# Kernel optimization log

Hardware: AMD Instinct MI355X
Metric: run time of the kernel (lower is better)

Reference implementation:

```python
import jax, jax.numpy as jnp
import numpy as np

B, L, DIM, H, HD = 2, 2048, 1024, 16, 64


def _rope_tables(L, hd):
    inv_freq = 1.0 / (10000.0 ** (np.arange(0, hd, 2, dtype=np.float32) / hd))
    t = np.arange(L, dtype=np.float32)
    freqs = np.outer(t, inv_freq)                 # [L, hd/2]
    emb = np.concatenate([freqs, freqs], axis=-1)  # [L, hd]
    return jnp.asarray(np.cos(emb)), jnp.asarray(np.sin(emb))


def setup_inputs() -> dict:
    key = jax.random.key(0)
    k1, k2, k3 = jax.random.split(key, 3)
    x = jax.random.normal(k1, (B, L, DIM), dtype=jnp.float32)
    cos, sin = _rope_tables(L, HD)
    w_qkv = jax.random.normal(k2, (DIM, 3 * H * HD), dtype=jnp.float32) * (DIM ** -0.5)
    w_out = jax.random.normal(k3, (H * HD, DIM), dtype=jnp.float32) * ((H * HD) ** -0.5)
    return {"x": x, "cos": cos, "sin": sin, "w_qkv": w_qkv, "w_out": w_out}


def _rotate_half(u):
    u1, u2 = jnp.split(u, 2, axis=-1)
    return jnp.concatenate([-u2, u1], axis=-1)


def _apply_rope(u, cos, sin):
    # u: [B, L, H, hd]; cos/sin: [L, hd]
    c = cos[None, :, None, :]
    s = sin[None, :, None, :]
    return u * c + _rotate_half(u) * s


def reference(x, cos, sin, w_qkv, w_out):
    b, l, _ = x.shape
    qkv = jnp.einsum('bld,de->ble', x, w_qkv).reshape(b, l, 3 * H, HD)
    q, k, v = jnp.split(qkv, 3, axis=2)          # each [B, L, H, hd]
    q = _apply_rope(q, cos, sin)
    k = _apply_rope(k, cos, sin)
    scale = HD ** -0.5                            # SDPA default scale
    scores = jnp.einsum('bqhd,bkhd->bhqk', q, k) * scale
    attn = jax.nn.softmax(scores, axis=-1)
    o = jnp.einsum('bhqk,bkhd->bqhd', attn, v).reshape(b, l, H * HD)
    return jnp.einsum('ble,ed->bld', o, w_out)
```

## Files before the change

### kernel.cpp

```cpp
#include <hip/hip_runtime.h>
#include <hip/hip_bf16.h>

#define BATCH 2
#define SEQ   2048
#define DIM   1024
#define NH    16
#define HD    64
#define K_DIM 1024

typedef __attribute__((ext_vector_type(8))) short short8;
typedef __attribute__((ext_vector_type(4))) short short4v;
typedef __attribute__((ext_vector_type(4))) float f32x4;
typedef unsigned short ushort_t;

__device__ __forceinline__ unsigned short f2b(float x) {
    unsigned int u = __float_as_uint(x);
    u += 0x7FFFu + ((u >> 16) & 1u);
    return (unsigned short)(u >> 16);
}

#define ASYNC_COPY16(gp, lp) \
    __builtin_amdgcn_global_load_lds((const __attribute__((address_space(1))) void*)(gp), \
                                     (__attribute__((address_space(3))) void*)(lp), 16, 0, 0)

__global__ __launch_bounds__(256)
void prep(const float* __restrict__ x, const float* __restrict__ w_qkv,
          const float* __restrict__ w_out, ushort_t* __restrict__ xb,
          ushort_t* __restrict__ wqb, ushort_t* __restrict__ wob)
{
    const int bid = blockIdx.x;
    if (bid < 1024) {
        constexpr int n4 = (BATCH * SEQ * DIM) / 4;
        int i = bid * 256 + threadIdx.x;
        for (; i < n4; i += 1024 * 256) {
            float4 v = ((const float4*)x)[i];
            short4v o;
            o[0] = (short)f2b(v.x); o[1] = (short)f2b(v.y);
            o[2] = (short)f2b(v.z); o[3] = (short)f2b(v.w);
            ((short4v*)xb)[i] = o;
        }
    } else {
        const int lane = threadIdx.x & 63;
        const float* src; ushort_t* dst; int N, job;
        if (bid < 2560) { src = w_qkv; dst = wqb; N = 3072; job = (bid - 1024) * 4 + (threadIdx.x >> 6); }
        else            { src = w_out; dst = wob; N = 1024; job = (bid - 2560) * 4 + (threadIdx.x >> 6); }
        const int jn = (N == 3072) ? (job % 48) : (job % 16);
        const int jk = (N == 3072) ? (job / 48) : (job / 16);
        const int n  = jn * 64 + lane;
        const int k0 = jk * 8;
        short8 o;
        #pragma unroll
        for (int j = 0; j < 8; ++j) o[j] = (short)f2b(src[(size_t)(k0 + j) * N + n]);
        *(short8*)(dst + (size_t)n * K_DIM + k0) = o;
    }
}

__device__ __forceinline__ void gemm_stage(const ushort_t* __restrict__ Ag,
                                           const ushort_t* __restrict__ Bg,
                                           ushort_t* As, ushort_t* Bs,
                                           int k0, int w, int r0, int c0)
{
    ASYNC_COPY16(Ag + (size_t)r0 * K_DIM + k0 + c0 * 8,        As + w * 512);
    ASYNC_COPY16(Ag + (size_t)(64 + r0) * K_DIM + k0 + c0 * 8, As + w * 512 + 2048);
    ASYNC_COPY16(Bg + (size_t)r0 * K_DIM + k0 + c0 * 8,        Bs + w * 512);
    ASYNC_COPY16(Bg + (size_t)(64 + r0) * K_DIM + k0 + c0 * 8, Bs + w * 512 + 2048);
}

__device__ __forceinline__ void mfma_gemm_tile(
    const ushort_t* __restrict__ Ag, const ushort_t* __restrict__ Bg,
    ushort_t (&As)[2][128 * 32], ushort_t (&Bs)[2][128 * 32], f32x4 acc[4][4])
{
    const int t = threadIdx.x;
    const int w = t >> 6, lane = t & 63;
    const int qd = lane >> 4, cl = lane & 15;
    const int p0 = w * 64 + lane;
    const int r0 = p0 >> 2;
    const int c0 = (p0 & 3) ^ (r0 & 3);

    gemm_stage(Ag, Bg, As[0], Bs[0], 0, w, r0, c0);

    for (int kt = 0; kt < K_DIM / 32; ++kt) {
        const int cur = kt & 1;
        __syncthreads();
        if (kt + 1 < K_DIM / 32)
            gemm_stage(Ag, Bg, As[cur ^ 1], Bs[cur ^ 1], (kt + 1) * 32, w, r0, c0);

        short8 af[4], bfr[4];
        #pragma unroll
        for (int rt = 0; rt < 4; ++rt) {
            const int row = (w >> 1) * 64 + rt * 16 + cl;
            af[rt] = *(const short8*)(As[cur] + row * 32 + ((qd ^ (row & 3)) * 8));
        }
        #pragma unroll
        for (int ct = 0; ct < 4; ++ct) {
            const int col = (w & 1) * 64 + ct * 16 + cl;
            bfr[ct] = *(const short8*)(Bs[cur] + col * 32 + ((qd ^ (col & 3)) * 8));
        }
        #pragma unroll
        for (int rt = 0; rt < 4; ++rt)
            #pragma unroll
            for (int ct = 0; ct < 4; ++ct)
                acc[rt][ct] = __builtin_amdgcn_mfma_f32_16x16x32_bf16(
                    af[rt], bfr[ct], acc[rt][ct], 0, 0, 0);
    }
}

__global__ __launch_bounds__(256, 3)
void gemm_qkv_mfma(const ushort_t* __restrict__ xb, const ushort_t* __restrict__ wqb,
                   ushort_t* __restrict__ qb, ushort_t* __restrict__ kb,
                   ushort_t* __restrict__ vt,
                   const float* __restrict__ cosb, const float* __restrict__ sinb)
{
    __shared__ __align__(16) ushort_t As[2][128 * 32];
    __shared__ __align__(16) ushort_t Bs[2][128 * 32];
    const int m0 = blockIdx.y * 128, n0 = blockIdx.x * 128;

    f32x4 acc[4][4];
    #pragma unroll
    for (int i = 0; i < 4; ++i)
        #pragma unroll
        for (int j = 0; j < 4; ++j)
            #pragma unroll
            for (int r = 0; r < 4; ++r) acc[i][j][r] = 0.f;

    mfma_gemm_tile(xb + (size_t)m0 * K_DIM, wqb + (size_t)n0 * K_DIM, As, Bs, acc);

    const int t = threadIdx.x, w = t >> 6, lane = t & 63;
    const int qd = lane >> 4, cl = lane & 15;
    const int b = m0 >> 11;
    const int lbase = (m0 & 2047) + (w >> 1) * 64;
    const int region = blockIdx.x >> 3;
    const int h = (blockIdx.x & 7) * 2 + (w & 1);

    if (region < 2) {
        ushort_t* dst = region ? kb : qb;
        const float sc = region ? 1.0f : 0.18033688011111234f;
        #pragma unroll
        for (int rt = 0; rt < 4; ++rt) {
            #pragma unroll
            for (int r = 0; r < 4; ++r) {
                const int l = lbase + rt * 16 + qd * 4 + r;
                const float c0 = cosb[l * HD + cl],      s0 = sinb[l * HD + cl];
                const float c1 = cosb[l * HD + 16 + cl], s1 = sinb[l * HD + 16 + cl];
                const float v0 = acc[rt][0][r] * c0 - acc[rt][2][r] * s0;
                const float v1 = acc[rt][1][r] * c1 - acc[rt][3][r] * s1;
                const float v2 = acc[rt][2][r] * c0 + acc[rt][0][r] * s0;
                const float v3 = acc[rt][3][r] * c1 + acc[rt][1][r] * s1;
                short4v o4;
                o4[0] = (short)f2b(v0 * sc);
                o4[1] = (short)f2b(v1 * sc);
                o4[2] = (short)f2b(v2 * sc);
                o4[3] = (short)f2b(v3 * sc);
                *(short4v*)(dst + (((size_t)b * NH + h) * SEQ + l) * HD + cl * 4) = o4;
            }
        }
    } else {
        #pragma unroll
        for (int rt = 0; rt < 4; ++rt)
            #pragma unroll
            for (int ct = 0; ct < 4; ++ct) {
                const int d = ct * 16 + cl;
                const int l = lbase + rt * 16 + qd * 4;
                short4v o4;
                #pragma unroll
                for (int r = 0; r < 4; ++r) o4[r] = (short)f2b(acc[rt][ct][r]);
                *(short4v*)(vt + (((size_t)b * NH + h) * HD + d) * SEQ + l) = o4;
            }
    }
}

__device__ __forceinline__ void go_stage(const ushort_t* __restrict__ Ag,
                                         const ushort_t* __restrict__ Bg,
                                         ushort_t* As, ushort_t* Bs,
                                         int k0, int w, int lane)
{
    #pragma unroll
    for (int j = 0; j < 2; ++j) {
        const int r = w * 32 + j * 16 + (lane >> 2);
        const int c = (lane & 3) ^ (r & 3);
        ASYNC_COPY16(Ag + (size_t)r * K_DIM + k0 + c * 8, As + (w * 128 + j * 64) * 8);
    }
    const int rb = w * 16 + (lane >> 2);
    const int cb = (lane & 3) ^ (rb & 3);
    ASYNC_COPY16(Bg + (size_t)rb * K_DIM + k0 + cb * 8, Bs + (w * 64) * 8);
}

__global__ __launch_bounds__(256, 3)
void gemm_out_mfma(const ushort_t* __restrict__ ob, const ushort_t* __restrict__ wob,
                   float* __restrict__ out)
{
    __shared__ __align__(16) ushort_t As[2][128 * 32];
    __shared__ __align__(16) ushort_t Bs[2][64 * 32];
    const int m0 = blockIdx.y * 128, n0 = blockIdx.x * 64;
    const int t = threadIdx.x;
    const int w = t >> 6, lane = t & 63;
    const int qd = lane >> 4, cl = lane & 15;
    const int wr = w >> 1, wc = w & 1;

    f32x4 acc[4][2];
    #pragma unroll
    for (int i = 0; i < 4; ++i)
        #pragma unroll
        for (int j = 0; j < 2; ++j)
            #pragma unroll
            for (int r = 0; r < 4; ++r) acc[i][j][r] = 0.f;

    const ushort_t* Ag = ob  + (size_t)m0 * K_DIM;
    const ushort_t* Bg = wob + (size_t)n0 * K_DIM;
    go_stage(Ag, Bg, As[0], Bs[0], 0, w, lane);

    for (int kt = 0; kt < K_DIM / 32; ++kt) {
        const int cur = kt & 1;
        __syncthreads();
        if (kt + 1 < K_DIM / 32)
            go_stage(Ag, Bg, As[cur ^ 1], Bs[cur ^ 1], (kt + 1) * 32, w, lane);

        short8 af[4], bfr[2];
        #pragma unroll
        for (int rt = 0; rt < 4; ++rt) {
            const int row = wr * 64 + rt * 16 + cl;
            af[rt] = *(const short8*)(As[cur] + row * 32 + ((qd ^ (row & 3)) * 8));
        }
        #pragma unroll
        for (int ct = 0; ct < 2; ++ct) {
            const int col = wc * 32 + ct * 16 + cl;
            bfr[ct] = *(const short8*)(Bs[cur] + col * 32 + ((qd ^ (col & 3)) * 8));
        }
        #pragma unroll
        for (int rt = 0; rt < 4; ++rt)
            #pragma unroll
            for (int ct = 0; ct < 2; ++ct)
                acc[rt][ct] = __builtin_amdgcn_mfma_f32_16x16x32_bf16(
                    af[rt], bfr[ct], acc[rt][ct], 0, 0, 0);
    }

    const int mbase = m0 + wr * 64, nbase = n0 + wc * 32;
    #pragma unroll
    for (int rt = 0; rt < 4; ++rt)
        #pragma unroll
        for (int ct = 0; ct < 2; ++ct)
            #pragma unroll
            for (int r = 0; r < 4; ++r)
                out[(size_t)(mbase + rt * 16 + qd * 4 + r) * DIM + nbase + ct * 16 + cl] =
                    acc[rt][ct][r];
}

__global__ __launch_bounds__(256, 3)
void attn_mfma(const ushort_t* __restrict__ qb, const ushort_t* __restrict__ kb,
               const ushort_t* __restrict__ vt, ushort_t* __restrict__ ob)
{
    const int h = blockIdx.x;
    const int b = blockIdx.y;
    const int qt = blockIdx.z;
    const int t = threadIdx.x;
    const int w = t >> 6, lane = t & 63;
    const int qd = lane >> 4, cl = lane & 15;
    constexpr int NT = SEQ / 64;

    __shared__ __align__(16) ushort_t Ks[2][64 * 64];
    __shared__ __align__(16) ushort_t Vs[2][64 * 64];
    __shared__ __align__(16) ushort_t P[4][2048];
    char* Pb = (char*)P[w];

    const size_t bh = (size_t)b * NH + h;
    const ushort_t* qbase = qb + (bh * SEQ + qt * 128 + w * 32) * HD;
    const ushort_t* kbase = kb + bh * SEQ * HD;
    const ushort_t* vbase = vt + bh * (size_t)HD * SEQ;

    const int p0 = w * 128 + lane;
    const int r0a = p0 >> 3,  c0a = (p0 & 7) ^ (r0a & 7);
    const int p1 = p0 + 64;
    const int r1a = p1 >> 3,  c1a = (p1 & 7) ^ (r1a & 7);
    const int ldsoff0 = (w * 128) * 8;
    const int ldsoff1 = (w * 128 + 64) * 8;

    short8 qf[2][2];
    #pragma unroll
    for (int nt = 0; nt < 2; ++nt)
        #pragma unroll
        for (int kh = 0; kh < 2; ++kh)
            qf[nt][kh] = *(const short8*)(qbase + (nt * 16 + cl) * HD + kh * 32 + qd * 8);

    f32x4 oaccT[4][2];
    float l_part[2] = {0.f, 0.f};
    #pragma unroll
    for (int dt = 0; dt < 4; ++dt)
        #pragma unroll
        for (int nt = 0; nt < 2; ++nt)
            #pragma unroll
            for (int r = 0; r < 4; ++r) oaccT[dt][nt][r] = 0.f;

    short8 pf_prev[2][2], vf_prev[4][2];
    #pragma unroll
    for (int nt = 0; nt < 2; ++nt)
        #pragma unroll
        for (int kh = 0; kh < 2; ++kh)
            #pragma unroll
            for (int e = 0; e < 8; ++e) pf_prev[nt][kh][e] = 0;
    #pragma unroll
    for (int dt = 0; dt < 4; ++dt)
        #pragma unroll
        for (int kh = 0; kh < 2; ++kh)
            #pragma unroll
            for (int e = 0; e < 8; ++e) vf_prev[dt][kh][e] = 0;

    {
        ASYNC_COPY16(kbase + (size_t)r0a * HD + c0a * 8,            (ushort_t*)Ks[0] + ldsoff0);
        ASYNC_COPY16(kbase + (size_t)r1a * HD + c1a * 8,            (ushort_t*)Ks[0] + ldsoff1);
        ASYNC_COPY16(vbase + (size_t)r0a * SEQ + c0a * 8,           (ushort_t*)Vs[0] + ldsoff0);
        ASYNC_COPY16(vbase + (size_t)r1a * SEQ + c1a * 8,           (ushort_t*)Vs[0] + ldsoff1);
    }

    for (int kt = 0; kt < NT; ++kt) {
        const int cur = kt & 1;
        __syncthreads();
        if (kt + 1 < NT) {
            const int g = kt + 1;
            ASYNC_COPY16(kbase + (size_t)(g * 64 + r0a) * HD + c0a * 8, (ushort_t*)Ks[cur ^ 1] + ldsoff0);
            ASYNC_COPY16(kbase + (size_t)(g * 64 + r1a) * HD + c1a * 8, (ushort_t*)Ks[cur ^ 1] + ldsoff1);
            ASYNC_COPY16(vbase + (size_t)r0a * SEQ + g * 64 + c0a * 8,  (ushort_t*)Vs[cur ^ 1] + ldsoff0);
            ASYNC_COPY16(vbase + (size_t)r1a * SEQ + g * 64 + c1a * 8,  (ushort_t*)Vs[cur ^ 1] + ldsoff1);
        }

        short8 kf[4][2], vf[4][2];
        #pragma unroll
        for (int mt = 0; mt < 4; ++mt)
            #pragma unroll
            for (int kh = 0; kh < 2; ++kh)
                kf[mt][kh] = *(const short8*)(Ks[cur] + ((mt * 16 + cl) * 8 + ((kh * 4 + qd) ^ (cl & 7))) * 8);
        #pragma unroll
        for (int dt = 0; dt < 4; ++dt)
            #pragma unroll
            for (int kh = 0; kh < 2; ++kh)
                vf[dt][kh] = *(const short8*)(Vs[cur] + ((dt * 16 + cl) * 8 + ((kh * 4 + qd) ^ (cl & 7))) * 8);

        f32x4 s[4][2];
        #pragma unroll
        for (int mt = 0; mt < 4; ++mt)
            #pragma unroll
            for (int nt = 0; nt < 2; ++nt)
                #pragma unroll
                for (int r = 0; r < 4; ++r) s[mt][nt][r] = 0.f;
        #pragma unroll
        for (int kh = 0; kh < 2; ++kh)
            #pragma unroll
            for (int mt = 0; mt < 4; ++mt)
                #pragma unroll
                for (int nt = 0; nt < 2; ++nt)
                    s[mt][nt] = __builtin_amdgcn_mfma_f32_16x16x32_bf16(
                        kf[mt][kh], qf[nt][kh], s[mt][nt], 0, 0, 0);

        #pragma unroll
        for (int kh = 0; kh < 2; ++kh)
            #pragma unroll
            for (int dt = 0; dt < 4; ++dt)
                #pragma unroll
                for (int nt = 0; nt < 2; ++nt)
                    oaccT[dt][nt] = __builtin_amdgcn_mfma_f32_16x16x32_bf16(
                        vf_prev[dt][kh], pf_prev[nt][kh], oaccT[dt][nt], 0, 0, 0);

        #pragma unroll
        for (int nt = 0; nt < 2; ++nt) {
            #pragma unroll
            for (int mt = 0; mt < 4; ++mt) {
                const float e0 = __builtin_amdgcn_exp2f(s[mt][nt][0]);
                const float e1 = __builtin_amdgcn_exp2f(s[mt][nt][1]);
                const float e2 = __builtin_amdgcn_exp2f(s[mt][nt][2]);
                const float e3 = __builtin_amdgcn_exp2f(s[mt][nt][3]);
                l_part[nt] += (e0 + e1) + (e2 + e3);
                union { __hip_bfloat162 h2[2]; unsigned long long u64; } pk;
                pk.h2[0] = __float22bfloat162_rn(make_float2(e0, e1));
                pk.h2[1] = __float22bfloat162_rn(make_float2(e2, e3));
                const int g = (mt * 2 + (qd >> 1)) ^ (cl & 7);
                *(unsigned long long*)(Pb + (nt * 16 + cl) * 128 + g * 16 + (qd & 1) * 8) = pk.u64;
            }
        }
        __builtin_amdgcn_wave_barrier();

        #pragma unroll
        for (int nt = 0; nt < 2; ++nt)
            #pragma unroll
            for (int kh = 0; kh < 2; ++kh)
                pf_prev[nt][kh] = *(const short8*)(Pb + (nt * 16 + cl) * 128 + (((kh * 4 + qd) ^ (cl & 7)) * 16));
        #pragma unroll
        for (int dt = 0; dt < 4; ++dt)
            #pragma unroll
            for (int kh = 0; kh < 2; ++kh)
                vf_prev[dt][kh] = vf[dt][kh];
    }

    #pragma unroll
    for (int kh = 0; kh < 2; ++kh)
        #pragma unroll
        for (int dt = 0; dt < 4; ++dt)
            #pragma unroll
            for (int nt = 0; nt < 2; ++nt)
                oaccT[dt][nt] = __builtin_amdgcn_mfma_f32_16x16x32_bf16(
                    vf_prev[dt][kh], pf_prev[nt][kh], oaccT[dt][nt], 0, 0, 0);

    #pragma unroll
    for (int nt = 0; nt < 2; ++nt) {
        float l = l_part[nt];
        l += __shfl_xor(l, 16);
        l += __shfl_xor(l, 32);
        const float inv = 1.0f / l;
        const int query = qt * 128 + w * 32 + nt * 16 + cl;
        ushort_t* op = ob + ((size_t)b * SEQ + query) * DIM + h * HD;
        #pragma unroll
        for (int dt = 0; dt < 4; ++dt) {
            short4v o4;
            #pragma unroll
            for (int r = 0; r < 4; ++r) o4[r] = (short)f2b(oaccT[dt][nt][r] * inv);
            *(short4v*)(op + dt * 16 + qd * 4) = o4;
        }
    }
}

extern "C" void kernel_launch(void* const* d_in, const int* in_sizes, int n_in,
                              void* d_out, int out_size, void* d_ws, size_t ws_size,
                              hipStream_t stream)
{
    const float* x     = (const float*)d_in[0];
    const float* cosb  = (const float*)d_in[1];
    const float* sinb  = (const float*)d_in[2];
    const float* w_qkv = (const float*)d_in[3];
    const float* w_out = (const float*)d_in[4];
    float* out = (float*)d_out;

    constexpr size_t MB = 1u << 20;
    char* ws = (char*)d_ws;
    ushort_t* qb  = (ushort_t*)(ws);
    ushort_t* kb  = (ushort_t*)(ws + 8 * MB);
    ushort_t* vt  = (ushort_t*)(ws + 16 * MB);
    ushort_t* wob = (ushort_t*)(ws + 24 * MB);
    ushort_t* ob  = (ushort_t*)(ws + 26 * MB);
    ushort_t* xb  = (ushort_t*)(ws + 34 * MB);
    ushort_t* wqb = (ushort_t*)(ws + 42 * MB);

    prep<<<3072, 256, 0, stream>>>(x, w_qkv, w_out, xb, wqb, wob);
    gemm_qkv_mfma<<<dim3(24, 32), 256, 0, stream>>>(xb, wqb, qb, kb, vt, cosb, sinb);
    attn_mfma<<<dim3(16, 2, 16), 256, 0, stream>>>(qb, kb, vt, ob);
    gemm_out_mfma<<<dim3(16, 32), 256, 0, stream>>>(ob, wob, out);
}
```

Before: 201.4 us.

## Repack softmax P via permlane swaps instead of LDS round-trip in attention

Removes the per-wave LDS scratch buffer used to transpose the bf16 probability tile into MFMA operand layout, and builds the operand registers directly with v_permlane32_swap and v_permlane16_swap cross-lane exchanges. This cuts LDS stores and loads plus a wave barrier per KV tile and lowers LDS usage. It also raises wave priority around the MFMA block and lowers the launch-bounds occupancy hint from 3 to 2, which gives the compiler more registers per thread but allows fewer resident blocks. If the permlane mapping does not exactly reproduce the old LDS layout, the attention output will be wrong.

```diff
diff --git a/kernel.cpp b/kernel.cpp
--- a/kernel.cpp
+++ b/kernel.cpp
@@ -245,7 +245,7 @@
                     acc[rt][ct][r];
 }
 
-__global__ __launch_bounds__(256, 3)
+__global__ __launch_bounds__(256, 2)
 void attn_mfma(const ushort_t* __restrict__ qb, const ushort_t* __restrict__ kb,
                const ushort_t* __restrict__ vt, ushort_t* __restrict__ ob)
 {
@@ -259,8 +259,6 @@
 
     __shared__ __align__(16) ushort_t Ks[2][64 * 64];
     __shared__ __align__(16) ushort_t Vs[2][64 * 64];
-    __shared__ __align__(16) ushort_t P[4][2048];
-    char* Pb = (char*)P[w];
 
     const size_t bh = (size_t)b * NH + h;
     const ushort_t* qbase = qb + (bh * SEQ + qt * 128 + w * 32) * HD;
@@ -341,6 +339,7 @@
             for (int nt = 0; nt < 2; ++nt)
                 #pragma unroll
                 for (int r = 0; r < 4; ++r) s[mt][nt][r] = 0.f;
+        __builtin_amdgcn_s_setprio(1);
         #pragma unroll
         for (int kh = 0; kh < 2; ++kh)
             #pragma unroll
@@ -358,9 +357,11 @@
                 for (int nt = 0; nt < 2; ++nt)
                     oaccT[dt][nt] = __builtin_amdgcn_mfma_f32_16x16x32_bf16(
                         vf_prev[dt][kh], pf_prev[nt][kh], oaccT[dt][nt], 0, 0, 0);
+        __builtin_amdgcn_s_setprio(0);
 
         #pragma unroll
         for (int nt = 0; nt < 2; ++nt) {
+            unsigned int wr[4][2];
             #pragma unroll
             for (int mt = 0; mt < 4; ++mt) {
                 const float e0 = __builtin_amdgcn_exp2f(s[mt][nt][0]);
@@ -368,20 +369,27 @@
                 const float e2 = __builtin_amdgcn_exp2f(s[mt][nt][2]);
                 const float e3 = __builtin_amdgcn_exp2f(s[mt][nt][3]);
                 l_part[nt] += (e0 + e1) + (e2 + e3);
-                union { __hip_bfloat162 h2[2]; unsigned long long u64; } pk;
-                pk.h2[0] = __float22bfloat162_rn(make_float2(e0, e1));
-                pk.h2[1] = __float22bfloat162_rn(make_float2(e2, e3));
-                const int g = (mt * 2 + (qd >> 1)) ^ (cl & 7);
-                *(unsigned long long*)(Pb + (nt * 16 + cl) * 128 + g * 16 + (qd & 1) * 8) = pk.u64;
+                union { __hip_bfloat162 h2; unsigned int u; } pk0, pk1;
+                pk0.h2 = __float22bfloat162_rn(make_float2(e0, e1));
+                pk1.h2 = __float22bfloat162_rn(make_float2(e2, e3));
+                wr[mt][0] = pk0.u;
+                wr[mt][1] = pk1.u;
             }
-        }
-        __builtin_amdgcn_wave_barrier();
-
-        #pragma unroll
-        for (int nt = 0; nt < 2; ++nt)
-            #pragma unroll
-            for (int kh = 0; kh < 2; ++kh)
-                pf_prev[nt][kh] = *(const short8*)(Pb + (nt * 16 + cl) * 128 + (((kh * 4 + qd) ^ (cl & 7)) * 16));
+            #pragma unroll
+            for (int kh = 0; kh < 2; ++kh) {
+                union { unsigned int u[4]; short8 s8; } pu;
+                #pragma unroll
+                for (int i = 0; i < 2; ++i) {
+                    unsigned int a  = wr[2 * kh][i];
+                    unsigned int bb = wr[2 * kh + 1][i];
+                    asm("v_permlane32_swap_b32 %0, %1" : "+v"(a), "+v"(bb));
+                    asm("v_permlane16_swap_b32 %0, %1" : "+v"(a), "+v"(bb));
+                    pu.u[i]     = a;
+                    pu.u[2 + i] = bb;
+                }
+                pf_prev[nt][kh] = pu.s8;
+            }
+        }
         #pragma unroll
         for (int dt = 0; dt < 4; ++dt)
             #pragma unroll
```

Result: faster. 191.0 us (-5.2%).

## Restructure attention pipeline with register-only P, MFMA row sums, and deeper K/V staging

Applied to the files above, without the earlier changes.

The attention kernel now stages K/V two 64-key tiles at a time into four LDS buffers and processes them in unrolled pairs. Exp results are kept in registers via permlane swaps instead of round-tripping through LDS, and softmax denominators are accumulated with an MFMA against a ones vector. The QK and PV MFMAs run at raised wave priority. The GEMM loops are unrolled by two with precomputed LDS fragment pointers to cut address arithmetic. These changes raise LDS and register use, so occupancy drops from three to two blocks per CU, and the tighter schedule is harder to verify as correct.

```diff
diff --git a/kernel.cpp b/kernel.cpp
--- a/kernel.cpp
+++ b/kernel.cpp
@@ -77,31 +77,53 @@
     const int r0 = p0 >> 2;
     const int c0 = (p0 & 3) ^ (r0 & 3);
 
+    const ushort_t* aB[4];
+    const ushort_t* bB[4];
+    #pragma unroll
+    for (int rt = 0; rt < 4; ++rt) {
+        const int row = (w >> 1) * 64 + rt * 16 + cl;
+        aB[rt] = As[0] + row * 32 + ((qd ^ (row & 3)) * 8);
+    }
+    #pragma unroll
+    for (int ct = 0; ct < 4; ++ct) {
+        const int col = (w & 1) * 64 + ct * 16 + cl;
+        bB[ct] = Bs[0] + col * 32 + ((qd ^ (col & 3)) * 8);
+    }
+
     gemm_stage(Ag, Bg, As[0], Bs[0], 0, w, r0, c0);
 
-    for (int kt = 0; kt < K_DIM / 32; ++kt) {
-        const int cur = kt & 1;
+    for (int kp = 0; kp < K_DIM / 64; ++kp) {
         __syncthreads();
-        if (kt + 1 < K_DIM / 32)
-            gemm_stage(Ag, Bg, As[cur ^ 1], Bs[cur ^ 1], (kt + 1) * 32, w, r0, c0);
-
-        short8 af[4], bfr[4];
-        #pragma unroll
-        for (int rt = 0; rt < 4; ++rt) {
-            const int row = (w >> 1) * 64 + rt * 16 + cl;
-            af[rt] = *(const short8*)(As[cur] + row * 32 + ((qd ^ (row & 3)) * 8));
-        }
-        #pragma unroll
-        for (int ct = 0; ct < 4; ++ct) {
-            const int col = (w & 1) * 64 + ct * 16 + cl;
-            bfr[ct] = *(const short8*)(Bs[cur] + col * 32 + ((qd ^ (col & 3)) * 8));
-        }
-        #pragma unroll
-        for (int rt = 0; rt < 4; ++rt)
-            #pragma unroll
-            for (int ct = 0; ct < 4; ++ct)
-                acc[rt][ct] = __builtin_amdgcn_mfma_f32_16x16x32_bf16(
-                    af[rt], bfr[ct], acc[rt][ct], 0, 0, 0);
+        gemm_stage(Ag, Bg, As[1], Bs[1], kp * 64 + 32, w, r0, c0);
+        {
+            short8 af[4], bfr[4];
+            #pragma unroll
+            for (int rt = 0; rt < 4; ++rt) af[rt] = *(const short8*)(aB[rt]);
+            #pragma unroll
+            for (int ct = 0; ct < 4; ++ct) bfr[ct] = *(const short8*)(bB[ct]);
+            #pragma unroll
+            for (int rt = 0; rt < 4; ++rt)
+                #pragma unroll
+                for (int ct = 0; ct < 4; ++ct)
+                    acc[rt][ct] = __builtin_amdgcn_mfma_f32_16x16x32_bf16(
+                        af[rt], bfr[ct], acc[rt][ct], 0, 0, 0);
+        }
+        __syncthreads();
+        if (kp + 1 < K_DIM / 64)
+            gemm_stage(Ag, Bg, As[0], Bs[0], kp * 64 + 64, w, r0, c0);
+        {
+            short8 af[4], bfr[4];
+            #pragma unroll
+            for (int rt = 0; rt < 4; ++rt) af[rt] = *(const short8*)(aB[rt] + 4096);
+            #pragma unroll
+            for (int ct = 0; ct < 4; ++ct) bfr[ct] = *(const short8*)(bB[ct] + 4096);
+            #pragma unroll
+            for (int rt = 0; rt < 4; ++rt)
+                #pragma unroll
+                for (int ct = 0; ct < 4; ++ct)
+                    acc[rt][ct] = __builtin_amdgcn_mfma_f32_16x16x32_bf16(
+                        af[rt], bfr[ct], acc[rt][ct], 0, 0, 0);
+        }
     }
 }
 
@@ -207,31 +229,54 @@
 
     const ushort_t* Ag = ob  + (size_t)m0 * K_DIM;
     const ushort_t* Bg = wob + (size_t)n0 * K_DIM;
+
+    const ushort_t* aB[4];
+    const ushort_t* bB[2];
+    #pragma unroll
+    for (int rt = 0; rt < 4; ++rt) {
+        const int row = wr * 64 + rt * 16 + cl;
+        aB[rt] = As[0] + row * 32 + ((qd ^ (row & 3)) * 8);
+    }
+    #pragma unroll
+    for (int ct = 0; ct < 2; ++ct) {
+        const int col = wc * 32 + ct * 16 + cl;
+        bB[ct] = Bs[0] + col * 32 + ((qd ^ (col & 3)) * 8);
+    }
+
     go_stage(Ag, Bg, As[0], Bs[0], 0, w, lane);
 
-    for (int kt = 0; kt < K_DIM / 32; ++kt) {
-        const int cur = kt & 1;
+    for (int kp = 0; kp < K_DIM / 64; ++kp) {
         __syncthreads();
-        if (kt + 1 < K_DIM / 32)
-            go_stage(Ag, Bg, As[cur ^ 1], Bs[cur ^ 1], (kt + 1) * 32, w, lane);
-
-        short8 af[4], bfr[2];
-        #pragma unroll
-        for (int rt = 0; rt < 4; ++rt) {
-            const int row = wr * 64 + rt * 16 + cl;
-            af[rt] = *(const short8*)(As[cur] + row * 32 + ((qd ^ (row & 3)) * 8));
-        }
-        #pragma unroll
-        for (int ct = 0; ct < 2; ++ct) {
-            const int col = wc * 32 + ct * 16 + cl;
-            bfr[ct] = *(const short8*)(Bs[cur] + col * 32 + ((qd ^ (col & 3)) * 8));
-        }
-        #pragma unroll
-        for (int rt = 0; rt < 4; ++rt)
-            #pragma unroll
-            for (int ct = 0; ct < 2; ++ct)
-                acc[rt][ct] = __builtin_amdgcn_mfma_f32_16x16x32_bf16(
-                    af[rt], bfr[ct], acc[rt][ct], 0, 0, 0);
+        go_stage(Ag, Bg, As[1], Bs[1], kp * 64 + 32, w, lane);
+        {
+            short8 af[4], bfr[2];
+            #pragma unroll
+            for (int rt = 0; rt < 4; ++rt) af[rt] = *(const short8*)(aB[rt]);
+            #pragma unroll
+            for (int ct = 0; ct < 2; ++ct) bfr[ct] = *(const short8*)(bB[ct]);
+            #pragma unroll
+            for (int rt = 0; rt < 4; ++rt)
+                #pragma unroll
+                for (int ct = 0; ct < 2; ++ct)
+                    acc[rt][ct] = __builtin_amdgcn_mfma_f32_16x16x32_bf16(
+                        af[rt], bfr[ct], acc[rt][ct], 0, 0, 0);
+        }
+        __syncthreads();
+        if (kp + 1 < K_DIM / 64)
+            go_stage(Ag, Bg, As[0], Bs[0], kp * 64 + 64, w, lane);
+        {
+            short8 af[4], bfr[2];
+            #pragma unroll
+            for (int rt = 0; rt < 4; ++rt) af[rt] = *(const short8*)(aB[rt] + 4096);
+            #pragma unroll
+            for (int ct = 0; ct < 2; ++ct) bfr[ct] = *(const short8*)(bB[ct] + 2048);
+            #pragma unroll
+            for (int rt = 0; rt < 4; ++rt)
+                #pragma unroll
+                for (int ct = 0; ct < 2; ++ct)
+                    acc[rt][ct] = __builtin_amdgcn_mfma_f32_16x16x32_bf16(
+                        af[rt], bfr[ct], acc[rt][ct], 0, 0, 0);
+        }
     }
 
     const int mbase = m0 + wr * 64, nbase = n0 + wc * 32;
@@ -245,7 +290,111 @@
                     acc[rt][ct][r];
 }
 
-__global__ __launch_bounds__(256, 3)
+#define QK_MFMA(kfv, sdst)                                                      \
+    _Pragma("unroll")                                                           \
+    for (int mt = 0; mt < 4; ++mt)                                              \
+        _Pragma("unroll")                                                       \
+        for (int nt = 0; nt < 2; ++nt)                                          \
+            sdst[mt][nt] = __builtin_amdgcn_mfma_f32_16x16x32_bf16(             \
+                kfv[mt][0], qf[nt][0], fz, 0, 0, 0);                            \
+    _Pragma("unroll")                                                           \
+    for (int mt = 0; mt < 4; ++mt)                                              \
+        _Pragma("unroll")                                                       \
+        for (int nt = 0; nt < 2; ++nt)                                          \
+            sdst[mt][nt] = __builtin_amdgcn_mfma_f32_16x16x32_bf16(             \
+                kfv[mt][1], qf[nt][1], sdst[mt][nt], 0, 0, 0);
+
+#define PV_MFMA(vfv, pfv)                                                       \
+    _Pragma("unroll")                                                           \
+    for (int kh = 0; kh < 2; ++kh)                                              \
+        _Pragma("unroll")                                                       \
+        for (int dt = 0; dt < 4; ++dt)                                          \
+            _Pragma("unroll")                                                   \
+            for (int nt = 0; nt < 2; ++nt)                                      \
+                oaccT[dt][nt] = __builtin_amdgcn_mfma_f32_16x16x32_bf16(        \
+                    vfv[dt][kh], pfv[nt][kh], oaccT[dt][nt], 0, 0, 0);
+
+#define L_MFMA(pfv)                                                             \
+    _Pragma("unroll")                                                           \
+    for (int kh = 0; kh < 2; ++kh)                                              \
+        _Pragma("unroll")                                                       \
+        for (int nt = 0; nt < 2; ++nt)                                          \
+            lacc[nt] = __builtin_amdgcn_mfma_f32_16x16x32_bf16(                 \
+                onesA, pfv[nt][kh], lacc[nt], 0, 0, 0);
+
+#define EXPPACK(sv, pfD)                                                        \
+    _Pragma("unroll")                                                           \
+    for (int nt = 0; nt < 2; ++nt) {                                            \
+        unsigned int wr2[4][2];                                                 \
+        _Pragma("unroll")                                                       \
+        for (int mt = 0; mt < 4; ++mt) {                                        \
+            const float e0 = __builtin_amdgcn_exp2f(sv[mt][nt][0]);             \
+            const float e1 = __builtin_amdgcn_exp2f(sv[mt][nt][1]);             \
+            const float e2 = __builtin_amdgcn_exp2f(sv[mt][nt][2]);             \
+            const float e3 = __builtin_amdgcn_exp2f(sv[mt][nt][3]);             \
+            union { __hip_bfloat162 h2; unsigned int u; } pk0, pk1;             \
+            pk0.h2 = __float22bfloat162_rn(make_float2(e0, e1));                \
+            pk1.h2 = __float22bfloat162_rn(make_float2(e2, e3));                \
+            wr2[mt][0] = pk0.u;                                                 \
+            wr2[mt][1] = pk1.u;                                                 \
+        }                                                                       \
+        _Pragma("unroll")                                                       \
+        for (int kh = 0; kh < 2; ++kh) {                                        \
+            union { unsigned int u[4]; short8 s8; } pu;                         \
+            _Pragma("unroll")                                                   \
+            for (int i = 0; i < 2; ++i) {                                       \
+                unsigned int a  = wr2[2 * kh][i];                               \
+                unsigned int bb = wr2[2 * kh + 1][i];                           \
+                asm("v_permlane32_swap_b32 %0, %1" : "+v"(a), "+v"(bb));        \
+                asm("v_permlane16_swap_b32 %0, %1" : "+v"(a), "+v"(bb));        \
+                pu.u[i]     = a;                                                \
+                pu.u[2 + i] = bb;                                               \
+            }                                                                   \
+            pfD[nt][kh] = pu.s8;                                                \
+        }                                                                       \
+    }
+
+#define PAIR_BODY(BOFF, pfC, vfC, pfP, vfP)                                     \
+    {                                                                           \
+        short8 kf[4][2], vfT[4][2], pfT[2][2];                                  \
+        f32x4 s[4][2];                                                          \
+                                                          \
+        _Pragma("unroll")                                                       \
+        for (int mt = 0; mt < 4; ++mt) {                                        \
+            kf[mt][0] = *(const short8*)(kb0 + (BOFF) + mt * 1024);             \
+            kf[mt][1] = *(const short8*)(kb1 + (BOFF) + mt * 1024);             \
+        }                                                                       \
+        _Pragma("unroll")                                                       \
+        for (int dt = 0; dt < 4; ++dt) {                                        \
+            vfT[dt][0] = *(const short8*)(vb0 + (BOFF) + dt * 1024);            \
+            vfT[dt][1] = *(const short8*)(vb1 + (BOFF) + dt * 1024);            \
+        }                                                                       \
+        __builtin_amdgcn_s_setprio(1);                                          \
+        QK_MFMA(kf, s)                                                          \
+        PV_MFMA(vfC, pfC)                                                       \
+        __builtin_amdgcn_s_setprio(0);                                          \
+        EXPPACK(s, pfT)                                                         \
+        L_MFMA(pfT)                                                             \
+                                                          \
+        _Pragma("unroll")                                                       \
+        for (int mt = 0; mt < 4; ++mt) {                                        \
+            kf[mt][0] = *(const short8*)(kb0 + (BOFF) + 4096 + mt * 1024);      \
+            kf[mt][1] = *(const short8*)(kb1 + (BOFF) + 4096 + mt * 1024);      \
+        }                                                                       \
+        _Pragma("unroll")                                                       \
+        for (int dt = 0; dt < 4; ++dt) {                                        \
+            vfP[dt][0] = *(const short8*)(vb0 + (BOFF) + 4096 + dt * 1024);     \
+            vfP[dt][1] = *(const short8*)(vb1 + (BOFF) + 4096 + dt * 1024);     \
+        }                                                                       \
+        __builtin_amdgcn_s_setprio(1);                                          \
+        QK_MFMA(kf, s)                                                          \
+        PV_MFMA(vfT, pfT)                                                       \
+        __builtin_amdgcn_s_setprio(0);                                          \
+        EXPPACK(s, pfP)                                                         \
+        L_MFMA(pfP)                                                             \
+    }
+
+__global__ __launch_bounds__(256, 2)
 void attn_mfma(const ushort_t* __restrict__ qb, const ushort_t* __restrict__ kb,
                const ushort_t* __restrict__ vt, ushort_t* __restrict__ ob)
 {
@@ -255,12 +404,9 @@
     const int t = threadIdx.x;
     const int w = t >> 6, lane = t & 63;
     const int qd = lane >> 4, cl = lane & 15;
-    constexpr int NT = SEQ / 64;
-
-    __shared__ __align__(16) ushort_t Ks[2][64 * 64];
-    __shared__ __align__(16) ushort_t Vs[2][64 * 64];
-    __shared__ __align__(16) ushort_t P[4][2048];
-    char* Pb = (char*)P[w];
+
+    __shared__ __align__(16) ushort_t Ks[4][64 * 64];
+    __shared__ __align__(16) ushort_t Vs[4][64 * 64];
 
     const size_t bh = (size_t)b * NH + h;
     const ushort_t* qbase = qb + (bh * SEQ + qt * 128 + w * 32) * HD;
@@ -274,6 +420,16 @@
     const int ldsoff0 = (w * 128) * 8;
     const int ldsoff1 = (w * 128 + 64) * 8;
 
+    const ushort_t* kg0 = kbase + (size_t)r0a * HD + c0a * 8;
+    const ushort_t* kg1 = kbase + (size_t)r1a * HD + c1a * 8;
+    const ushort_t* vg0 = vbase + (size_t)r0a * SEQ + c0a * 8;
+    const ushort_t* vg1 = vbase + (size_t)r1a * SEQ + c1a * 8;
+
+    const int lo0 = (cl * 8 + (qd ^ (cl & 7))) * 8;
+    const int lo1 = (cl * 8 + ((4 + qd) ^ (cl & 7))) * 8;
+    const ushort_t* kb0 = Ks[0] + lo0; const ushort_t* kb1 = Ks[0] + lo1;
+    const ushort_t* vb0 = Vs[0] + lo0; const ushort_t* vb1 = Vs[0] + lo1;
+
     short8 qf[2][2];
     #pragma unroll
     for (int nt = 0; nt < 2; ++nt)
@@ -281,129 +437,85 @@
         for (int kh = 0; kh < 2; ++kh)
             qf[nt][kh] = *(const short8*)(qbase + (nt * 16 + cl) * HD + kh * 32 + qd * 8);
 
+    const f32x4 fz = {0.f, 0.f, 0.f, 0.f};
+    short8 onesA;
+    #pragma unroll
+    for (int e = 0; e < 8; ++e) onesA[e] = (short)0x3F80;
+
     f32x4 oaccT[4][2];
-    float l_part[2] = {0.f, 0.f};
+    f32x4 lacc[2];
     #pragma unroll
     for (int dt = 0; dt < 4; ++dt)
         #pragma unroll
         for (int nt = 0; nt < 2; ++nt)
             #pragma unroll
             for (int r = 0; r < 4; ++r) oaccT[dt][nt][r] = 0.f;
-
-    short8 pf_prev[2][2], vf_prev[4][2];
     #pragma unroll
     for (int nt = 0; nt < 2; ++nt)
         #pragma unroll
+        for (int r = 0; r < 4; ++r) lacc[nt][r] = 0.f;
+
+    short8 pf01[2][2], vf01[4][2], pf23[2][2], vf23[4][2];
+    #pragma unroll
+    for (int nt = 0; nt < 2; ++nt)
+        #pragma unroll
         for (int kh = 0; kh < 2; ++kh)
             #pragma unroll
-            for (int e = 0; e < 8; ++e) pf_prev[nt][kh][e] = 0;
+            for (int e = 0; e < 8; ++e) pf23[nt][kh][e] = 0;
     #pragma unroll
     for (int dt = 0; dt < 4; ++dt)
         #pragma unroll
         for (int kh = 0; kh < 2; ++kh)
             #pragma unroll
-            for (int e = 0; e < 8; ++e) vf_prev[dt][kh][e] = 0;
+            for (int e = 0; e < 8; ++e) vf23[dt][kh][e] = 0;
 
     {
-        ASYNC_COPY16(kbase + (size_t)r0a * HD + c0a * 8,            (ushort_t*)Ks[0] + ldsoff0);
-        ASYNC_COPY16(kbase + (size_t)r1a * HD + c1a * 8,            (ushort_t*)Ks[0] + ldsoff1);
-        ASYNC_COPY16(vbase + (size_t)r0a * SEQ + c0a * 8,           (ushort_t*)Vs[0] + ldsoff0);
-        ASYNC_COPY16(vbase + (size_t)r1a * SEQ + c1a * 8,           (ushort_t*)Vs[0] + ldsoff1);
-    }
-
-    for (int kt = 0; kt < NT; ++kt) {
-        const int cur = kt & 1;
+        ASYNC_COPY16(kg0,            (ushort_t*)Ks[0] + ldsoff0);
+        ASYNC_COPY16(kg1,            (ushort_t*)Ks[0] + ldsoff1);
+        ASYNC_COPY16(vg0,            (ushort_t*)Vs[0] + ldsoff0);
+        ASYNC_COPY16(vg1,            (ushort_t*)Vs[0] + ldsoff1);
+        ASYNC_COPY16(kg0 + 64 * HD,  (ushort_t*)Ks[1] + ldsoff0);
+        ASYNC_COPY16(kg1 + 64 * HD,  (ushort_t*)Ks[1] + ldsoff1);
+        ASYNC_COPY16(vg0 + 64,       (ushort_t*)Vs[1] + ldsoff0);
+        ASYNC_COPY16(vg1 + 64,       (ushort_t*)Vs[1] + ldsoff1);
+        kg0 += 128 * HD; kg1 += 128 * HD; vg0 += 128; vg1 += 128;
+    }
+
+    for (int q8 = 0; q8 < 8; ++q8) {
         __syncthreads();
-        if (kt + 1 < NT) {
-            const int g = kt + 1;
-            ASYNC_COPY16(kbase + (size_t)(g * 64 + r0a) * HD + c0a * 8, (ushort_t*)Ks[cur ^ 1] + ldsoff0);
-            ASYNC_COPY16(kbase + (size_t)(g * 64 + r1a) * HD + c1a * 8, (ushort_t*)Ks[cur ^ 1] + ldsoff1);
-            ASYNC_COPY16(vbase + (size_t)r0a * SEQ + g * 64 + c0a * 8,  (ushort_t*)Vs[cur ^ 1] + ldsoff0);
-            ASYNC_COPY16(vbase + (size_t)r1a * SEQ + g * 64 + c1a * 8,  (ushort_t*)Vs[cur ^ 1] + ldsoff1);
-        }
-
-        short8 kf[4][2], vf[4][2];
-        #pragma unroll
-        for (int mt = 0; mt < 4; ++mt)
-            #pragma unroll
-            for (int kh = 0; kh < 2; ++kh)
-                kf[mt][kh] = *(const short8*)(Ks[cur] + ((mt * 16 + cl) * 8 + ((kh * 4 + qd) ^ (cl & 7))) * 8);
-        #pragma unroll
-        for (int dt = 0; dt < 4; ++dt)
-            #pragma unroll
-            for (int kh = 0; kh < 2; ++kh)
-                vf[dt][kh] = *(const short8*)(Vs[cur] + ((dt * 16 + cl) * 8 + ((kh * 4 + qd) ^ (cl & 7))) * 8);
-
-        f32x4 s[4][2];
-        #pragma unroll
-        for (int mt = 0; mt < 4; ++mt)
-            #pragma unroll
-            for (int nt = 0; nt < 2; ++nt)
-                #pragma unroll
-                for (int r = 0; r < 4; ++r) s[mt][nt][r] = 0.f;
-        #pragma unroll
-        for (int kh = 0; kh < 2; ++kh)
-            #pragma unroll
-            for (int mt = 0; mt < 4; ++mt)
-                #pragma unroll
-                for (int nt = 0; nt < 2; ++nt)
-                    s[mt][nt] = __builtin_amdgcn_mfma_f32_16x16x32_bf16(
-                        kf[mt][kh], qf[nt][kh], s[mt][nt], 0, 0, 0);
-
-        #pragma unroll
-        for (int kh = 0; kh < 2; ++kh)
-            #pragma unroll
-            for (int dt = 0; dt < 4; ++dt)
-                #pragma unroll
-                for (int nt = 0; nt < 2; ++nt)
-                    oaccT[dt][nt] = __builtin_amdgcn_mfma_f32_16x16x32_bf16(
-                        vf_prev[dt][kh], pf_prev[nt][kh], oaccT[dt][nt], 0, 0, 0);
-
-        #pragma unroll
-        for (int nt = 0; nt < 2; ++nt) {
-            #pragma unroll
-            for (int mt = 0; mt < 4; ++mt) {
-                const float e0 = __builtin_amdgcn_exp2f(s[mt][nt][0]);
-                const float e1 = __builtin_amdgcn_exp2f(s[mt][nt][1]);
-                const float e2 = __builtin_amdgcn_exp2f(s[mt][nt][2]);
-                const float e3 = __builtin_amdgcn_exp2f(s[mt][nt][3]);
-                l_part[nt] += (e0 + e1) + (e2 + e3);
-                union { __hip_bfloat162 h2[2]; unsigned long long u64; } pk;
-                pk.h2[0] = __float22bfloat162_rn(make_float2(e0, e1));
-                pk.h2[1] = __float22bfloat162_rn(make_float2(e2, e3));
-                const int g = (mt * 2 + (qd >> 1)) ^ (cl & 7);
-                *(unsigned long long*)(Pb + (nt * 16 + cl) * 128 + g * 16 + (qd & 1) * 8) = pk.u64;
-            }
-        }
-        __builtin_amdgcn_wave_barrier();
-
-        #pragma unroll
-        for (int nt = 0; nt < 2; ++nt)
-            #pragma unroll
-            for (int kh = 0; kh < 2; ++kh)
-                pf_prev[nt][kh] = *(const short8*)(Pb + (nt * 16 + cl) * 128 + (((kh * 4 + qd) ^ (cl & 7)) * 16));
-        #pragma unroll
-        for (int dt = 0; dt < 4; ++dt)
-            #pragma unroll
-            for (int kh = 0; kh < 2; ++kh)
-                vf_prev[dt][kh] = vf[dt][kh];
-    }
-
-    #pragma unroll
-    for (int kh = 0; kh < 2; ++kh)
-        #pragma unroll
-        for (int dt = 0; dt < 4; ++dt)
-            #pragma unroll
-            for (int nt = 0; nt < 2; ++nt)
-                oaccT[dt][nt] = __builtin_amdgcn_mfma_f32_16x16x32_bf16(
-                    vf_prev[dt][kh], pf_prev[nt][kh], oaccT[dt][nt], 0, 0, 0);
+        {
+            ASYNC_COPY16(kg0,            (ushort_t*)Ks[2] + ldsoff0);
+            ASYNC_COPY16(kg1,            (ushort_t*)Ks[2] + ldsoff1);
+            ASYNC_COPY16(vg0,            (ushort_t*)Vs[2] + ldsoff0);
+            ASYNC_COPY16(vg1,            (ushort_t*)Vs[2] + ldsoff1);
+            ASYNC_COPY16(kg0 + 64 * HD,  (ushort_t*)Ks[3] + ldsoff0);
+            ASYNC_COPY16(kg1 + 64 * HD,  (ushort_t*)Ks[3] + ldsoff1);
+            ASYNC_COPY16(vg0 + 64,       (ushort_t*)Vs[3] + ldsoff0);
+            ASYNC_COPY16(vg1 + 64,       (ushort_t*)Vs[3] + ldsoff1);
+            kg0 += 128 * HD; kg1 += 128 * HD; vg0 += 128; vg1 += 128;
+        }
+        PAIR_BODY(0, pf23, vf23, pf01, vf01)
+
+        __syncthreads();
+        if (q8 + 1 < 8) {
+            ASYNC_COPY16(kg0,            (ushort_t*)Ks[0] + ldsoff0);
+            ASYNC_COPY16(kg1,            (ushort_t*)Ks[0] + ldsoff1);
+            ASYNC_COPY16(vg0,            (ushort_t*)Vs[0] + ldsoff0);
+            ASYNC_COPY16(vg1,            (ushort_t*)Vs[0] + ldsoff1);
+            ASYNC_COPY16(kg0 + 64 * HD,  (ushort_t*)Ks[1] + ldsoff0);
+            ASYNC_COPY16(kg1 + 64 * HD,  (ushort_t*)Ks[1] + ldsoff1);
+            ASYNC_COPY16(vg0 + 64,       (ushort_t*)Vs[1] + ldsoff0);
+            ASYNC_COPY16(vg1 + 64,       (ushort_t*)Vs[1] + ldsoff1);
+            kg0 += 128 * HD; kg1 += 128 * HD; vg0 += 128; vg1 += 128;
+        }
+        PAIR_BODY(8192, pf01, vf01, pf23, vf23)
+    }
+
+    PV_MFMA(vf23, pf23)
 
     #pragma unroll
     for (int nt = 0; nt < 2; ++nt) {
-        float l = l_part[nt];
-        l += __shfl_xor(l, 16);
-        l += __shfl_xor(l, 32);
-        const float inv = 1.0f / l;
+        const float inv = 1.0f / lacc[nt][0];
         const int query = qt * 128 + w * 32 + nt * 16 + cl;
         ushort_t* op = ob + ((size_t)b * SEQ + query) * DIM + h * HD;
         #pragma unroll
```

Result: faster. 190.8 us (-5.3%).
